# Kernel optimization log

Hardware: AMD Instinct MI355X
Metric: run time of the kernel (lower is better)

## Reference

```python
import jax, jax.numpy as jnp
import numpy as np

N, IN, H, C, E = 20000, 256, 256, 16, 640000

def sage_conv(x, edge_index, W_l, b_l, W_r):
    # PyG SAGEConv (aggr='mean', root_weight=True):
    # out = lin_l(mean_{j in N(i)} x_j) + lin_r(x_i)
    src, dst = edge_index[0], edge_index[1]
    n = x.shape[0]
    msgs = x[src]                                            # [E, d] irregular gather
    agg = jax.ops.segment_sum(msgs, dst, num_segments=n)     # [N, d]
    deg = jax.ops.segment_sum(jnp.ones((msgs.shape[0],), x.dtype), dst, num_segments=n)
    agg = agg / jnp.maximum(deg, 1.0)[:, None]               # mean aggregation
    return agg @ W_l + b_l + x @ W_r


def setup_inputs() -> dict:
    key = jax.random.key(0)
    ks = jax.random.split(key, 10)
    s = lambda k, fi, fo: jax.random.normal(k, (fi, fo), jnp.float32) / np.sqrt(fi)
    return {
        "x": jax.random.normal(ks[0], (N, IN), jnp.float32),
        "edge_index": jax.random.randint(ks[1], (2, E), 0, N, jnp.int64),
        "W1l": s(ks[2], IN, H), "b1": jnp.zeros((H,), jnp.float32), "W1r": s(ks[3], IN, H),
        "W2l": s(ks[4], H, H),  "b2": jnp.zeros((H,), jnp.float32), "W2r": s(ks[5], H, H),
        "Wc": s(ks[6], H, C),   "bc": jnp.zeros((C,), jnp.float32),
    }


def reference(x, edge_index, W1l, b1, W1r, W2l, b2, W2r, Wc, bc):
    h = sage_conv(x, edge_index, W1l, b1, W1r)
    h = jax.nn.relu(h)                    # dropout is identity in eval mode
    z = sage_conv(h, edge_index, W2l, b2, W2r)
    return z @ Wc + bc                    # classifier logits [N, C]
```

## Files before the change

kernel.cpp:

```cpp
#include <hip/hip_runtime.h>
#include <hip/hip_bf16.h>


#define FEAT 256
#define NCLS 16
#define ZPAD 264
#define CAP  128

typedef __bf16 bf16x8 __attribute__((ext_vector_type(8)));
typedef __bf16 bf16x4 __attribute__((ext_vector_type(4)));
typedef float  f32x4  __attribute__((ext_vector_type(4)));
typedef float  f32x2  __attribute__((ext_vector_type(2)));
typedef unsigned int uint4v __attribute__((ext_vector_type(4)));


__global__ void combo_kernel(const float* __restrict__ x,
                             const float* __restrict__ W1l, const float* __restrict__ W1r,
                             const float* __restrict__ W2l, const float* __restrict__ W2r,
                             const float* __restrict__ Wc, const float* __restrict__ b2,
                             const float* __restrict__ bc,
                             const int* __restrict__ src, const int* __restrict__ dst,
                             __bf16* __restrict__ xb, unsigned char* __restrict__ x8,
                             __bf16* __restrict__ W1lT, __bf16* __restrict__ W1rT,
                             __bf16* __restrict__ WaT, __bf16* __restrict__ WbT,
                             float* __restrict__ bc2,
                             int* __restrict__ cnt, int* __restrict__ bucket,
                             int n4, int E, int nb_cvt) {
    int t = threadIdx.x;
    int bx = blockIdx.x;
    if (bx < nb_cvt) {
        int i = bx * 256 + t;
        if (i < n4) {
            f32x4 v = ((const f32x4*)x)[i];
            bf16x4 o;
            #pragma unroll
            for (int j = 0; j < 4; ++j) o[j] = (__bf16)v[j];
            ((bf16x4*)xb)[i] = o;
            int pk = 0;
            pk = __builtin_amdgcn_cvt_pk_fp8_f32(v[0], v[1], pk, false);
            pk = __builtin_amdgcn_cvt_pk_fp8_f32(v[2], v[3], pk, true);
            ((int*)x8)[i] = pk;
        }
    } else if (bx < nb_cvt + 512) {
        int b = bx - nb_cvt;
        int w = b >> 8, nn = b & 255;
        const float* W = w ? W1r : W1l;
        __bf16* WT = w ? W1rT : W1lT;
        WT[nn * FEAT + t] = (__bf16)W[t * FEAT + nn];
    } else if (bx < nb_cvt + 512 + 32) {
        int b = bx - nb_cvt - 512;
        int c = b & 15;
        const float* W = (b < 16) ? W2l : W2r;
        __bf16* WT = (b < 16) ? WaT : WbT;
        float s = 0.f;
        #pragma unroll 4
        for (int m = 0; m < FEAT; ++m)
            s += W[t * FEAT + m] * Wc[m * NCLS + c];
        WT[c * FEAT + t] = (__bf16)s;
    } else if (bx == nb_cvt + 512 + 32) {
        if (t < NCLS) {
            float s = 0.f;
            for (int k = 0; k < FEAT; ++k) s += b2[k] * Wc[k * NCLS + t];
            bc2[t] = s + bc[t];
        }
    } else {
        int e = (bx - nb_cvt - 512 - 33) * 256 + t;
        if (e < E) {
            int d = dst[e];
            int p = atomicAdd(&cnt[d], 1);
            if (p < CAP) bucket[d * CAP + p] = src[e];
        }
    }
}


__global__ __launch_bounds__(256) void agg_fp8_kernel(
    const unsigned char* __restrict__ t8, const int* __restrict__ cnt,
    const int* __restrict__ bucket, __bf16* __restrict__ out, int n)
{
    int wave = threadIdx.x >> 6;
    int node = blockIdx.x * 4 + wave;
    if (node >= n) return;
    int lane = threadIdx.x & 63;
    int quad = lane >> 4, l16 = lane & 15;
    int c = cnt[node];
    int deg = c < CAP ? c : CAP;
    const int* lst = bucket + node * CAP;

    f32x4 s0[4], s1[4];
    #pragma unroll
    for (int w = 0; w < 4; ++w) { s0[w] = (f32x4){0.f,0.f,0.f,0.f}; s1[w] = (f32x4){0.f,0.f,0.f,0.f}; }

    int e = quad;
    for (; e + 4 < deg; e += 8) {
        int j0 = lst[e], j1 = lst[e + 4];
        uint4v u0 = *(const uint4v*)(t8 + (size_t)j0 * FEAT + l16 * 16);
        uint4v u1 = *(const uint4v*)(t8 + (size_t)j1 * FEAT + l16 * 16);
        #pragma unroll
        for (int w = 0; w < 4; ++w) {
            f32x2 lo0 = __builtin_amdgcn_cvt_pk_f32_fp8(u0[w], false);
            f32x2 hi0 = __builtin_amdgcn_cvt_pk_f32_fp8(u0[w], true);
            s0[w][0] += lo0[0]; s0[w][1] += lo0[1]; s0[w][2] += hi0[0]; s0[w][3] += hi0[1];
            f32x2 lo1 = __builtin_amdgcn_cvt_pk_f32_fp8(u1[w], false);
            f32x2 hi1 = __builtin_amdgcn_cvt_pk_f32_fp8(u1[w], true);
            s1[w][0] += lo1[0]; s1[w][1] += lo1[1]; s1[w][2] += hi1[0]; s1[w][3] += hi1[1];
        }
    }
    if (e < deg) {
        int j = lst[e];
        uint4v u = *(const uint4v*)(t8 + (size_t)j * FEAT + l16 * 16);
        #pragma unroll
        for (int w = 0; w < 4; ++w) {
            f32x2 lo = __builtin_amdgcn_cvt_pk_f32_fp8(u[w], false);
            f32x2 hi = __builtin_amdgcn_cvt_pk_f32_fp8(u[w], true);
            s0[w][0] += lo[0]; s0[w][1] += lo[1]; s0[w][2] += hi[0]; s0[w][3] += hi[1];
        }
    }

    #pragma unroll
    for (int w = 0; w < 4; ++w)
        #pragma unroll
        for (int j = 0; j < 4; ++j) {
            float v = s0[w][j] + s1[w][j];
            v += __shfl_xor(v, 16, 64);
            v += __shfl_xor(v, 32, 64);
            s0[w][j] = v;
        }

    float inv = (c > 0) ? 1.0f / (float)c : 0.0f;
    bf16x4 o;
    #pragma unroll
    for (int j = 0; j < 4; ++j) o[j] = (__bf16)(s0[quad][j] * inv);
    *(bf16x4*)(out + (size_t)node * FEAT + l16 * 16 + quad * 4) = o;
}


__global__ __launch_bounds__(256) void gemm1_kernel(
    const __bf16* __restrict__ A1, const __bf16* __restrict__ A2,
    const __bf16* __restrict__ B1T, const __bf16* __restrict__ B2T,
    const float* __restrict__ bias, __bf16* __restrict__ hb, int M)
{
    __shared__ __align__(16) __bf16 tile[32][ZPAD];

    int m0   = blockIdx.x * 32;
    int lane = threadIdx.x & 63;
    int wave = threadIdx.x >> 6;
    int l16  = lane & 15, quad = lane >> 4;

    f32x4 acc[2][4];
    #pragma unroll
    for (int a = 0; a < 2; ++a)
        #pragma unroll
        for (int b = 0; b < 4; ++b) acc[a][b] = (f32x4){0.f, 0.f, 0.f, 0.f};

    int arow[2];
    #pragma unroll
    for (int mt = 0; mt < 2; ++mt) {
        int r = m0 + mt * 16 + l16;
        arow[mt] = (r < M) ? r : (M - 1);
    }
    int nbase = wave * 64;

    for (int pass = 0; pass < 2; ++pass) {
        const __bf16* A  = pass ? A2 : A1;
        const __bf16* BT = pass ? B2T : B1T;
        #pragma unroll 2
        for (int kk = 0; kk < 8; ++kk) {
            int k0 = kk * 32 + quad * 8;
            bf16x8 af[2], bfm[4];
            #pragma unroll
            for (int mt = 0; mt < 2; ++mt)
                af[mt] = *(const bf16x8*)(A + (size_t)arow[mt] * FEAT + k0);
            #pragma unroll
            for (int nt = 0; nt < 4; ++nt)
                bfm[nt] = *(const bf16x8*)(BT + (size_t)(nbase + nt * 16 + l16) * FEAT + k0);
            #pragma unroll
            for (int mt = 0; mt < 2; ++mt)
                #pragma unroll
                for (int nt = 0; nt < 4; ++nt)
                    acc[mt][nt] = __builtin_amdgcn_mfma_f32_16x16x32_bf16(
                        af[mt], bfm[nt], acc[mt][nt], 0, 0, 0);
        }
    }

    #pragma unroll
    for (int nt = 0; nt < 4; ++nt) {
        int col = nbase + nt * 16 + l16;
        float bv = bias[col];
        #pragma unroll
        for (int mt = 0; mt < 2; ++mt) {
            int lr = mt * 16 + quad * 4;
            #pragma unroll
            for (int r = 0; r < 4; ++r) {
                float v = acc[mt][nt][r] + bv;
                tile[lr + r][col] = (__bf16)(v > 0.f ? v : 0.f);
            }
        }
    }
    __syncthreads();

    int row = threadIdx.x >> 3;
    int c0  = (threadIdx.x & 7) * 32;
    int grow = m0 + row;
    if (grow < M) {
        #pragma unroll
        for (int i = 0; i < 4; ++i)
            *(bf16x8*)(hb + (size_t)grow * FEAT + c0 + i * 8) =
                *(const bf16x8*)(&tile[row][c0 + i * 8]);
    }
}


__global__ __launch_bounds__(256) void gemm_pq_kernel(
    const __bf16* __restrict__ hb, const __bf16* __restrict__ WaT,
    const __bf16* __restrict__ WbT, const float* __restrict__ bc2,
    __bf16* __restrict__ pb, float* __restrict__ q, int M)
{
    int lane = threadIdx.x & 63, wave = threadIdx.x >> 6;
    int l16 = lane & 15, quad = lane >> 4;
    int m0 = blockIdx.x * 64 + wave * 16;
    int arow = m0 + l16;
    if (arow >= M) arow = M - 1;

    f32x4 ap = {0.f, 0.f, 0.f, 0.f}, aq = {0.f, 0.f, 0.f, 0.f};
    #pragma unroll
    for (int kk = 0; kk < 8; ++kk) {
        int k0 = kk * 32 + quad * 8;
        bf16x8 a  = *(const bf16x8*)(hb + (size_t)arow * FEAT + k0);
        bf16x8 ba = *(const bf16x8*)(WaT + (size_t)l16 * FEAT + k0);
        bf16x8 bb = *(const bf16x8*)(WbT + (size_t)l16 * FEAT + k0);
        ap = __builtin_amdgcn_mfma_f32_16x16x32_bf16(a, ba, ap, 0, 0, 0);
        aq = __builtin_amdgcn_mfma_f32_16x16x32_bf16(a, bb, aq, 0, 0, 0);
    }
    float qb = bc2[l16];
    #pragma unroll
    for (int r = 0; r < 4; ++r) {
        int row = m0 + quad * 4 + r;
        if (row < M) {
            pb[(size_t)row * NCLS + l16] = (__bf16)ap[r];
            q[(size_t)row * NCLS + l16] = aq[r] + qb;
        }
    }
}


__global__ __launch_bounds__(256) void agg_out_kernel(
    const __bf16* __restrict__ pb, const float* __restrict__ q,
    const int* __restrict__ cnt, const int* __restrict__ bucket,
    float* __restrict__ out, int n)
{
    int wave = threadIdx.x >> 6;
    int node = blockIdx.x * 4 + wave;
    if (node >= n) return;
    int lane = threadIdx.x & 63;
    int quad = lane >> 4, l16 = lane & 15;
    int c = cnt[node];
    int deg = c < CAP ? c : CAP;
    const int* lst = bucket + node * CAP;

    float s0 = 0.f, s1 = 0.f;
    int e = quad;
    for (; e + 4 < deg; e += 8) {
        int j0 = lst[e], j1 = lst[e + 4];
        s0 += (float)pb[(size_t)j0 * NCLS + l16];
        s1 += (float)pb[(size_t)j1 * NCLS + l16];
    }
    if (e < deg) s0 += (float)pb[(size_t)lst[e] * NCLS + l16];

    float v = s0 + s1;
    v += __shfl_xor(v, 16, 64);
    v += __shfl_xor(v, 32, 64);

    if (quad == 0) {
        float inv = (c > 0) ? 1.0f / (float)c : 0.0f;
        out[(size_t)node * NCLS + l16] = v * inv + q[(size_t)node * NCLS + l16];
    }
}


extern "C" void kernel_launch(void* const* d_in, const int* in_sizes, int n_in,
                              void* d_out, int out_size, void* d_ws, size_t ws_size,
                              hipStream_t stream) {
    const float* x   = (const float*)d_in[0];
    const int*   ei  = (const int*)d_in[1];
    const float* W1l = (const float*)d_in[2];
    const float* b1  = (const float*)d_in[3];
    const float* W1r = (const float*)d_in[4];
    const float* W2l = (const float*)d_in[5];
    const float* b2  = (const float*)d_in[6];
    const float* W2r = (const float*)d_in[7];
    const float* Wc  = (const float*)d_in[8];
    const float* bc  = (const float*)d_in[9];
    float* out = (float*)d_out;

    const int n = in_sizes[0] / FEAT;
    const int E = in_sizes[1] / 2;
    const int* srcp = ei;
    const int* dstp = ei + E;

    char* p = (char*)d_ws;
    auto alloc = [&](size_t bytes) { char* r = p; p += (bytes + 511) & ~511ull; return r; };
    int* cnt       = (int*)alloc((size_t)n * 4);
    int* bucket    = (int*)alloc((size_t)n * CAP * 4);
    __bf16* W1lT   = (__bf16*)alloc((size_t)FEAT * FEAT * 2);
    __bf16* W1rT   = (__bf16*)alloc((size_t)FEAT * FEAT * 2);
    __bf16* WaT    = (__bf16*)alloc((size_t)NCLS * FEAT * 2);
    __bf16* WbT    = (__bf16*)alloc((size_t)NCLS * FEAT * 2);
    float*  bc2    = (float*)alloc((size_t)NCLS * 4);
    __bf16* xb     = (__bf16*)alloc((size_t)n * FEAT * 2);
    unsigned char* x8 = (unsigned char*)alloc((size_t)n * FEAT);
    __bf16* aggb   = (__bf16*)alloc((size_t)n * FEAT * 2);
    __bf16* hb     = (__bf16*)alloc((size_t)n * FEAT * 2);
    __bf16* pb     = (__bf16*)alloc((size_t)n * NCLS * 2);
    float*  qb     = (float*)alloc((size_t)n * NCLS * 4);

    int n4 = n * FEAT / 4;
    int nb_cvt = (n4 + 255) / 256;
    int nb_edge = (E + 255) / 256;

    hipMemsetAsync(cnt, 0, (size_t)n * 4, stream);

    combo_kernel<<<nb_cvt + 512 + 32 + 1 + nb_edge, 256, 0, stream>>>(
        x, W1l, W1r, W2l, W2r, Wc, b2, bc, srcp, dstp,
        xb, x8, W1lT, W1rT, WaT, WbT, bc2, cnt, bucket, n4, E, nb_cvt);

    agg_fp8_kernel<<<(n + 3) / 4, 256, 0, stream>>>(x8, cnt, bucket, aggb, n);
    gemm1_kernel<<<(n + 31) / 32, 256, 0, stream>>>(aggb, xb, W1lT, W1rT, b1, hb, n);

    gemm_pq_kernel<<<(n + 63) / 64, 256, 0, stream>>>(hb, WaT, WbT, bc2, pb, qb, n);
    agg_out_kernel<<<(n + 3) / 4, 256, 0, stream>>>(pb, qb, cnt, bucket, out, n);
}
```

Measured before the change: 214.7 us.

## Fuse layer-2 projection into gemm1 epilogue and shrink adjacency bucket to 16-bit

The layer-1 GEMM now keeps the relu'd hidden tile in shared memory and immediately projects it onto the folded layer-2/classifier weights, writing pb and q directly. This removes the hb round trip through global memory and one kernel launch. The neighbour bucket now stores 16-bit source indices, halving its footprint and gather bandwidth, which depends on N being below 65536. The edge-scatter blocks also handle two edges per thread using vector loads.

New measurement: 204.3 us, median of 2. 4.8% less time.

```diff
diff --git a/kernel.cpp b/kernel.cpp
--- a/kernel.cpp
+++ b/kernel.cpp
@@ -24,7 +24,7 @@
                              __bf16* __restrict__ W1lT, __bf16* __restrict__ W1rT,
                              __bf16* __restrict__ WaT, __bf16* __restrict__ WbT,
                              float* __restrict__ bc2,
-                             int* __restrict__ cnt, int* __restrict__ bucket,
+                             int* __restrict__ cnt, unsigned short* __restrict__ bucket,
                              int n4, int E, int nb_cvt) {
     int t = threadIdx.x;
     int bx = blockIdx.x;
@@ -64,11 +64,17 @@
             bc2[t] = s + bc[t];
         }
     } else {
-        int e = (bx - nb_cvt - 512 - 33) * 256 + t;
-        if (e < E) {
-            int d = dst[e];
-            int p = atomicAdd(&cnt[d], 1);
-            if (p < CAP) bucket[d * CAP + p] = src[e];
+        int idx = (bx - nb_cvt - 512 - 33) * 256 + t;
+        int e2 = idx * 2;
+        if (e2 < E) {
+            int2 sv = *(const int2*)(src + e2);
+            int2 dv = *(const int2*)(dst + e2);
+            int p0 = atomicAdd(&cnt[dv.x], 1);
+            if (p0 < CAP) bucket[dv.x * CAP + p0] = (unsigned short)sv.x;
+            if (e2 + 1 < E) {
+                int p1 = atomicAdd(&cnt[dv.y], 1);
+                if (p1 < CAP) bucket[dv.y * CAP + p1] = (unsigned short)sv.y;
+            }
         }
     }
 }
@@ -76,7 +82,7 @@
 
 __global__ __launch_bounds__(256) void agg_fp8_kernel(
     const unsigned char* __restrict__ t8, const int* __restrict__ cnt,
-    const int* __restrict__ bucket, __bf16* __restrict__ out, int n)
+    const unsigned short* __restrict__ bucket, __bf16* __restrict__ out, int n)
 {
     int wave = threadIdx.x >> 6;
     int node = blockIdx.x * 4 + wave;
@@ -85,7 +91,7 @@
     int quad = lane >> 4, l16 = lane & 15;
     int c = cnt[node];
     int deg = c < CAP ? c : CAP;
-    const int* lst = bucket + node * CAP;
+    const unsigned short* lst = bucket + node * CAP;
 
     f32x4 s0[4], s1[4];
     #pragma unroll
@@ -138,7 +144,10 @@
 __global__ __launch_bounds__(256) void gemm1_kernel(
     const __bf16* __restrict__ A1, const __bf16* __restrict__ A2,
     const __bf16* __restrict__ B1T, const __bf16* __restrict__ B2T,
-    const float* __restrict__ bias, __bf16* __restrict__ hb, int M)
+    const float* __restrict__ bias,
+    const __bf16* __restrict__ WaT, const __bf16* __restrict__ WbT,
+    const float* __restrict__ bc2,
+    __bf16* __restrict__ pb, float* __restrict__ q, int M)
 {
     __shared__ __align__(16) __bf16 tile[32][ZPAD];
 
@@ -199,46 +208,26 @@
     }
     __syncthreads();
 
-    int row = threadIdx.x >> 3;
-    int c0  = (threadIdx.x & 7) * 32;
-    int grow = m0 + row;
-    if (grow < M) {
-        #pragma unroll
-        for (int i = 0; i < 4; ++i)
-            *(bf16x8*)(hb + (size_t)grow * FEAT + c0 + i * 8) =
-                *(const bf16x8*)(&tile[row][c0 + i * 8]);
-    }
-}
-
-
-__global__ __launch_bounds__(256) void gemm_pq_kernel(
-    const __bf16* __restrict__ hb, const __bf16* __restrict__ WaT,
-    const __bf16* __restrict__ WbT, const float* __restrict__ bc2,
-    __bf16* __restrict__ pb, float* __restrict__ q, int M)
-{
-    int lane = threadIdx.x & 63, wave = threadIdx.x >> 6;
-    int l16 = lane & 15, quad = lane >> 4;
-    int m0 = blockIdx.x * 64 + wave * 16;
-    int arow = m0 + l16;
-    if (arow >= M) arow = M - 1;
-
-    f32x4 ap = {0.f, 0.f, 0.f, 0.f}, aq = {0.f, 0.f, 0.f, 0.f};
-    #pragma unroll
-    for (int kk = 0; kk < 8; ++kk) {
-        int k0 = kk * 32 + quad * 8;
-        bf16x8 a  = *(const bf16x8*)(hb + (size_t)arow * FEAT + k0);
-        bf16x8 ba = *(const bf16x8*)(WaT + (size_t)l16 * FEAT + k0);
-        bf16x8 bb = *(const bf16x8*)(WbT + (size_t)l16 * FEAT + k0);
-        ap = __builtin_amdgcn_mfma_f32_16x16x32_bf16(a, ba, ap, 0, 0, 0);
-        aq = __builtin_amdgcn_mfma_f32_16x16x32_bf16(a, bb, aq, 0, 0, 0);
-    }
-    float qb = bc2[l16];
-    #pragma unroll
-    for (int r = 0; r < 4; ++r) {
-        int row = m0 + quad * 4 + r;
-        if (row < M) {
-            pb[(size_t)row * NCLS + l16] = (__bf16)ap[r];
-            q[(size_t)row * NCLS + l16] = aq[r] + qb;
+    if (wave < 2) {
+        int lr = wave * 16 + l16;
+        f32x4 ap = {0.f, 0.f, 0.f, 0.f}, aq = {0.f, 0.f, 0.f, 0.f};
+        #pragma unroll
+        for (int kk = 0; kk < 8; ++kk) {
+            int k0 = kk * 32 + quad * 8;
+            bf16x8 a  = *(const bf16x8*)(&tile[lr][k0]);
+            bf16x8 ba = *(const bf16x8*)(WaT + (size_t)l16 * FEAT + k0);
+            bf16x8 bb = *(const bf16x8*)(WbT + (size_t)l16 * FEAT + k0);
+            ap = __builtin_amdgcn_mfma_f32_16x16x32_bf16(a, ba, ap, 0, 0, 0);
+            aq = __builtin_amdgcn_mfma_f32_16x16x32_bf16(a, bb, aq, 0, 0, 0);
+        }
+        float qv = bc2[l16];
+        #pragma unroll
+        for (int r = 0; r < 4; ++r) {
+            int row = m0 + wave * 16 + quad * 4 + r;
+            if (row < M) {
+                pb[(size_t)row * NCLS + l16] = (__bf16)ap[r];
+                q[(size_t)row * NCLS + l16] = aq[r] + qv;
+            }
         }
     }
 }
@@ -246,7 +235,7 @@
 
 __global__ __launch_bounds__(256) void agg_out_kernel(
     const __bf16* __restrict__ pb, const float* __restrict__ q,
-    const int* __restrict__ cnt, const int* __restrict__ bucket,
+    const int* __restrict__ cnt, const unsigned short* __restrict__ bucket,
     float* __restrict__ out, int n)
 {
     int wave = threadIdx.x >> 6;
@@ -256,7 +245,7 @@
     int quad = lane >> 4, l16 = lane & 15;
     int c = cnt[node];
     int deg = c < CAP ? c : CAP;
-    const int* lst = bucket + node * CAP;
+    const unsigned short* lst = bucket + node * CAP;
 
     float s0 = 0.f, s1 = 0.f;
     int e = quad;
@@ -301,7 +290,7 @@
     char* p = (char*)d_ws;
     auto alloc = [&](size_t bytes) { char* r = p; p += (bytes + 511) & ~511ull; return r; };
     int* cnt       = (int*)alloc((size_t)n * 4);
-    int* bucket    = (int*)alloc((size_t)n * CAP * 4);
+    unsigned short* bucket = (unsigned short*)alloc((size_t)n * CAP * 2);
     __bf16* W1lT   = (__bf16*)alloc((size_t)FEAT * FEAT * 2);
     __bf16* W1rT   = (__bf16*)alloc((size_t)FEAT * FEAT * 2);
     __bf16* WaT    = (__bf16*)alloc((size_t)NCLS * FEAT * 2);
@@ -310,13 +299,12 @@
     __bf16* xb     = (__bf16*)alloc((size_t)n * FEAT * 2);
     unsigned char* x8 = (unsigned char*)alloc((size_t)n * FEAT);
     __bf16* aggb   = (__bf16*)alloc((size_t)n * FEAT * 2);
-    __bf16* hb     = (__bf16*)alloc((size_t)n * FEAT * 2);
     __bf16* pb     = (__bf16*)alloc((size_t)n * NCLS * 2);
     float*  qb     = (float*)alloc((size_t)n * NCLS * 4);
 
     int n4 = n * FEAT / 4;
     int nb_cvt = (n4 + 255) / 256;
-    int nb_edge = (E + 255) / 256;
+    int nb_edge = (E + 511) / 512;
 
     hipMemsetAsync(cnt, 0, (size_t)n * 4, stream);
 
@@ -325,8 +313,8 @@
         xb, x8, W1lT, W1rT, WaT, WbT, bc2, cnt, bucket, n4, E, nb_cvt);
 
     agg_fp8_kernel<<<(n + 3) / 4, 256, 0, stream>>>(x8, cnt, bucket, aggb, n);
-    gemm1_kernel<<<(n + 31) / 32, 256, 0, stream>>>(aggb, xb, W1lT, W1rT, b1, hb, n);
-
-    gemm_pq_kernel<<<(n + 63) / 64, 256, 0, stream>>>(hb, WaT, WbT, bc2, pb, qb, n);
+    gemm1_kernel<<<(n + 31) / 32, 256, 0, stream>>>(aggb, xb, W1lT, W1rT, b1,
+                                                    WaT, WbT, bc2, pb, qb, n);
+
     agg_out_kernel<<<(n + 3) / 4, 256, 0, stream>>>(pb, qb, cnt, bucket, out, n);
 }
```
